# Kernel tuning notes

Hardware: AMD Instinct MI355X
Metric: run time of the kernel (lower is better)

## Reference

```python
import jax, jax.numpy as jnp
import numpy as np

N = 100_000      # n_nodes
E = 1_000_000    # n_edges (avg degree 10)
DIN = 64
DOUT = 64


def setup_inputs() -> dict:
    key = jax.random.key(0)
    k1, k2, k3, k4 = jax.random.split(key, 4)
    x = jax.random.normal(k1, (N, DIN), dtype=jnp.float32)
    edge_index = jax.random.randint(k2, (2, E), 0, N, dtype=jnp.int32)
    # GCNConv linear weight (glorot-ish scale) and bias
    W = jax.random.normal(k3, (DIN, DOUT), dtype=jnp.float32) * (1.0 / np.sqrt(DIN))
    b = jax.random.normal(k4, (DOUT,), dtype=jnp.float32) * 0.01
    return {"x": x, "edge_index": edge_index, "W": W, "b": b}


def reference(x, edge_index, W, b):
    n = x.shape[0]
    # linear transform first (PyG GCNConv: x = self.lin(x))
    h = x @ W  # [N, DOUT]
    # add self-loops
    loop = jnp.arange(n, dtype=edge_index.dtype)
    row = jnp.concatenate([edge_index[0], loop])  # source j
    col = jnp.concatenate([edge_index[1], loop])  # target i
    # symmetric normalization: deg computed on target index (PyG gcn_norm)
    deg = jax.ops.segment_sum(jnp.ones(row.shape[0], dtype=h.dtype), col, num_segments=n)
    dinv = jnp.where(deg > 0, jax.lax.rsqrt(deg), 0.0)
    norm = dinv[row] * dinv[col]  # [E+N]
    # gather source features, scale, scatter-add to targets
    out = jax.ops.segment_sum(norm[:, None] * h[row], col, num_segments=n)
    out = out + b
    # dropout is identity in eval mode; act = relu
    return jax.nn.relu(out)
```

## Files before the change

### kernel.cpp

```cpp
#include <hip/hip_runtime.h>
#include <hip/hip_bf16.h>

#define F 64
#define BK 128
#define CAP 4096
#define PA_BLOCKS 256

typedef __attribute__((ext_vector_type(8))) short bf16x8;
typedef __attribute__((ext_vector_type(4))) float f32x4;

static __device__ inline short f2bf_bits(float f) {
    union { __hip_bfloat16 b; short s; } cv;
    cv.b = __float2bfloat16(f);
    return cv.s;
}

static __device__ inline void bf8_add(uint4 u, float* a) {
    a[0] += __uint_as_float(u.x << 16);
    a[1] += __uint_as_float(u.x & 0xffff0000u);
    a[2] += __uint_as_float(u.y << 16);
    a[3] += __uint_as_float(u.y & 0xffff0000u);
    a[4] += __uint_as_float(u.z << 16);
    a[5] += __uint_as_float(u.z & 0xffff0000u);
    a[6] += __uint_as_float(u.w << 16);
    a[7] += __uint_as_float(u.w & 0xffff0000u);
}

__global__ void gemm_kernel(const float* __restrict__ x, const float* __restrict__ W,
                            __hip_bfloat16* __restrict__ h, int* __restrict__ bcursor,
                            int n) {
    __shared__ short Wb[F * F];
    int tid = threadIdx.x;
    if (blockIdx.x == 0) {
        for (int i = tid; i < 1024; i += 256) bcursor[i] = 0;
    }
    for (int i = tid; i < F * F; i += 256) Wb[i] = f2bf_bits(W[i]);
    __syncthreads();
    int lane = tid & 63;
    int wv = tid >> 6;
    int quad = lane >> 4;
    int l16 = lane & 15;

    bf16x8 bfr[2][4];
#pragma unroll
    for (int ks = 0; ks < 2; ++ks)
#pragma unroll
        for (int nb = 0; nb < 4; ++nb) {
            bf16x8 f;
#pragma unroll
            for (int j = 0; j < 8; ++j)
                f[j] = Wb[(ks * 32 + quad * 8 + j) * F + nb * 16 + l16];
            bfr[ks][nb] = f;
        }

    int blockbase = blockIdx.x * 256;
#pragma unroll
    for (int mt = 0; mt < 4; ++mt) {
        int trow = blockbase + (wv * 4 + mt) * 16;
        int ar = trow + l16;
        bf16x8 af0, af1;
        if (ar < n) {
            const float* xr = x + (size_t)ar * F + quad * 8;
            float4 v0 = ((const float4*)xr)[0];
            float4 v1 = ((const float4*)xr)[1];
            float4 v2 = ((const float4*)(xr + 32))[0];
            float4 v3 = ((const float4*)(xr + 32))[1];
            af0[0] = f2bf_bits(v0.x); af0[1] = f2bf_bits(v0.y);
            af0[2] = f2bf_bits(v0.z); af0[3] = f2bf_bits(v0.w);
            af0[4] = f2bf_bits(v1.x); af0[5] = f2bf_bits(v1.y);
            af0[6] = f2bf_bits(v1.z); af0[7] = f2bf_bits(v1.w);
            af1[0] = f2bf_bits(v2.x); af1[1] = f2bf_bits(v2.y);
            af1[2] = f2bf_bits(v2.z); af1[3] = f2bf_bits(v2.w);
            af1[4] = f2bf_bits(v3.x); af1[5] = f2bf_bits(v3.y);
            af1[6] = f2bf_bits(v3.z); af1[7] = f2bf_bits(v3.w);
        } else {
            af0 = (bf16x8)0; af1 = (bf16x8)0;
        }
        f32x4 acc[4];
#pragma unroll
        for (int nb = 0; nb < 4; ++nb) {
            acc[nb] = (f32x4)0.f;
            acc[nb] = __builtin_amdgcn_mfma_f32_16x16x32_bf16(af0, bfr[0][nb], acc[nb], 0, 0, 0);
            acc[nb] = __builtin_amdgcn_mfma_f32_16x16x32_bf16(af1, bfr[1][nb], acc[nb], 0, 0, 0);
        }
#pragma unroll
        for (int nb = 0; nb < 4; ++nb)
#pragma unroll
            for (int r = 0; r < 4; ++r) {
                int grow = trow + quad * 4 + r;
                if (grow < n)
                    h[(size_t)grow * F + nb * 16 + l16] = __float2bfloat16(acc[nb][r]);
            }
    }
}

__global__ void passA_kernel(const int* __restrict__ row, const int* __restrict__ col,
                             int* __restrict__ bcursor, unsigned* __restrict__ bin,
                             int e, int K, int chunk) {
    __shared__ int lh[1024];
    __shared__ int lbase[1024];
    int tid = threadIdx.x;
    int s = blockIdx.x * chunk;
    int lim = s + chunk;
    if (lim > e) lim = e;
    for (int i = tid; i < K; i += 256) lh[i] = 0;
    __syncthreads();
    for (int i = s + tid; i < lim; i += 256) atomicAdd(&lh[col[i] >> 7], 1);
    __syncthreads();
    for (int i = tid; i < K; i += 256) {
        int c = lh[i];
        lbase[i] = c ? atomicAdd(&bcursor[i], c) : 0;
        lh[i] = 0;
    }
    __syncthreads();
    for (int i = s + tid; i < lim; i += 256) {
        int d = col[i];
        int bkt = d >> 7;
        int off = lbase[bkt] + atomicAdd(&lh[bkt], 1);
        if (off < CAP)
            bin[(size_t)bkt * CAP + off] = ((unsigned)row[i] << 7) | ((unsigned)d & 127u);
    }
}

__global__ void passB_kernel(const unsigned* __restrict__ bin, const int* __restrict__ bcursor,
                             int* __restrict__ csr, int4* __restrict__ rng4,
                             __hip_bfloat16* __restrict__ h, int n) {
    __shared__ int lcnt[BK];
    __shared__ int lcur[BK];
    __shared__ int sc[BK];
    __shared__ float sdinv[BK];
    int tid = threadIdx.x;
    int b = blockIdx.x;
    int base = b << 7;
    int s = b * CAP;
    int cnt_all = min(bcursor[b], CAP);
    int e2 = s + cnt_all;
    if (tid < BK) lcnt[tid] = 0;
    __syncthreads();
    for (int p = s + tid; p < e2; p += 256) atomicAdd(&lcnt[bin[p] & 127u], 1);
    __syncthreads();
    if (tid < BK) sc[tid] = lcnt[tid];
    __syncthreads();
    for (int off = 1; off < BK; off <<= 1) {
        int t = (tid < BK && tid >= off) ? sc[tid - off] : 0;
        __syncthreads();
        if (tid < BK) sc[tid] += t;
        __syncthreads();
    }
    if (tid < BK) {
        int cnt = lcnt[tid];
        int lstart = sc[tid] - cnt;
        lcur[tid] = lstart;
        int node = base + tid;
        if (node < n) {
            int gs = s + lstart;
            float di = rsqrtf((float)(cnt + 1));
            rng4[node] = make_int4(gs, gs + cnt, __float_as_int(di), 0);
            sdinv[tid] = di;
        }
    }
    __syncthreads();
    for (int p = s + tid; p < e2; p += 256) {
        unsigned u = bin[p];
        int ld = (int)(u & 127u);
        int src = (int)(u >> 7);
        int pos = s + atomicAdd(&lcur[ld], 1);
        csr[pos] = src;
    }
    int lim = BK * F;
    for (int idx = tid; idx < lim; idx += 256) {
        int node = base + (idx >> 6);
        if (node < n) {
            float di = sdinv[idx >> 6];
            size_t off = (size_t)node * F + (idx & 63);
            h[off] = __float2bfloat16(di * __bfloat162float(h[off]));
        }
    }
}

__global__ void gather_kernel(const __hip_bfloat16* __restrict__ h,
                              const int* __restrict__ csr,
                              const int4* __restrict__ rng4,
                              const float* __restrict__ b,
                              float* __restrict__ out, int n) {
    int gid = blockIdx.x * 256 + threadIdx.x;
    int i = gid >> 3;
    if (i >= n) return;
    int cl = gid & 7;
    const uint4* h8 = (const uint4*)h;
    int4 r4 = rng4[i];
    int p = r4.x, pend = r4.y;
    float di = __int_as_float(r4.z);
    float acc[8] = {0.f, 0.f, 0.f, 0.f, 0.f, 0.f, 0.f, 0.f};
    bf8_add(h8[(size_t)i * 8 + cl], acc);
    for (; p + 4 <= pend; p += 4) {
        int s0 = csr[p];     int s1 = csr[p + 1];
        int s2 = csr[p + 2]; int s3 = csr[p + 3];
        uint4 u0 = h8[(size_t)s0 * 8 + cl];
        uint4 u1 = h8[(size_t)s1 * 8 + cl];
        uint4 u2 = h8[(size_t)s2 * 8 + cl];
        uint4 u3 = h8[(size_t)s3 * 8 + cl];
        bf8_add(u0, acc);
        bf8_add(u1, acc);
        bf8_add(u2, acc);
        bf8_add(u3, acc);
    }
    for (; p < pend; ++p) bf8_add(h8[(size_t)csr[p] * 8 + cl], acc);
    float4 b0 = ((const float4*)b)[cl * 2];
    float4 b1 = ((const float4*)b)[cl * 2 + 1];
    float4 r0, r1;
    r0.x = di * acc[0] + b0.x; r0.y = di * acc[1] + b0.y;
    r0.z = di * acc[2] + b0.z; r0.w = di * acc[3] + b0.w;
    r1.x = di * acc[4] + b1.x; r1.y = di * acc[5] + b1.y;
    r1.z = di * acc[6] + b1.z; r1.w = di * acc[7] + b1.w;
    r0.x = r0.x > 0.f ? r0.x : 0.f; r0.y = r0.y > 0.f ? r0.y : 0.f;
    r0.z = r0.z > 0.f ? r0.z : 0.f; r0.w = r0.w > 0.f ? r0.w : 0.f;
    r1.x = r1.x > 0.f ? r1.x : 0.f; r1.y = r1.y > 0.f ? r1.y : 0.f;
    r1.z = r1.z > 0.f ? r1.z : 0.f; r1.w = r1.w > 0.f ? r1.w : 0.f;
    ((float4*)out)[(size_t)i * 16 + cl * 2] = r0;
    ((float4*)out)[(size_t)i * 16 + cl * 2 + 1] = r1;
}

extern "C" void kernel_launch(void* const* d_in, const int* in_sizes, int n_in,
                              void* d_out, int out_size, void* d_ws, size_t ws_size,
                              hipStream_t stream) {
    const float* x = (const float*)d_in[0];
    const int* ei  = (const int*)d_in[1];
    const float* W = (const float*)d_in[2];
    const float* b = (const float*)d_in[3];
    float* out = (float*)d_out;

    int n = in_sizes[0] / F;
    int e = in_sizes[1] / 2;
    const int* row = ei;
    const int* col = ei + e;
    int K = (n + BK - 1) / BK;

    __hip_bfloat16* h = (__hip_bfloat16*)d_ws;
    unsigned* bin = (unsigned*)((char*)d_ws + (size_t)n * F * 2);
    int* csr      = (int*)(bin + (size_t)K * CAP);
    int4* rng4    = (int4*)(csr + (size_t)K * CAP);
    int* bcursor  = (int*)(rng4 + n);

    gemm_kernel<<<(n + 255) / 256, 256, 0, stream>>>(x, W, h, bcursor, n);

    int chunk = (e + PA_BLOCKS - 1) / PA_BLOCKS;
    passA_kernel<<<PA_BLOCKS, 256, 0, stream>>>(row, col, bcursor, bin, e, K, chunk);

    passB_kernel<<<K, 256, 0, stream>>>(bin, bcursor, csr, rng4, h, n);

    gather_kernel<<<((size_t)n * 8 + 255) / 256, 256, 0, stream>>>(
        h, csr, rng4, b, out, n);
}
```

Measured before the change: 151.9 us.

## Merge GEMM with binning pass and replace CSR build with LDS-atomic bucket scatter

GEMM blocks and edge-binning blocks now run inside one launch as heterogeneous blocks, and the cursor reset moves to a memset. The CSR construction pass is removed. A small per-bucket kernel computes dinv, and a per-bucket gather kernel accumulates dinv-weighted neighbor features directly into a padded shared-memory tile with float atomics. This drops the CSR write/read and the in-place rescale of h. The cost is heavy LDS atomic traffic (8 atomics per thread per edge), an extra global dinv lookup per edge, and only K≈782 blocks with large LDS use in the gather stage.

```diff
diff --git a/kernel.cpp b/kernel.cpp
--- a/kernel.cpp
+++ b/kernel.cpp
@@ -5,6 +5,7 @@
 #define BK 128
 #define CAP 4096
 #define PA_BLOCKS 256
+#define STRIDE 65
 
 typedef __attribute__((ext_vector_type(8))) short bf16x8;
 typedef __attribute__((ext_vector_type(4))) float f32x4;
@@ -15,210 +16,168 @@
     return cv.s;
 }
 
-static __device__ inline void bf8_add(uint4 u, float* a) {
-    a[0] += __uint_as_float(u.x << 16);
-    a[1] += __uint_as_float(u.x & 0xffff0000u);
-    a[2] += __uint_as_float(u.y << 16);
-    a[3] += __uint_as_float(u.y & 0xffff0000u);
-    a[4] += __uint_as_float(u.z << 16);
-    a[5] += __uint_as_float(u.z & 0xffff0000u);
-    a[6] += __uint_as_float(u.w << 16);
-    a[7] += __uint_as_float(u.w & 0xffff0000u);
-}
-
-__global__ void gemm_kernel(const float* __restrict__ x, const float* __restrict__ W,
-                            __hip_bfloat16* __restrict__ h, int* __restrict__ bcursor,
-                            int n) {
-    __shared__ short Wb[F * F];
+__global__ void __launch_bounds__(256)
+k1_kernel(const float* __restrict__ x, const float* __restrict__ W,
+          __hip_bfloat16* __restrict__ h,
+          const int* __restrict__ row, const int* __restrict__ col,
+          int* __restrict__ bcursor, unsigned* __restrict__ bin,
+          int n, int e, int ngemm, int K, int chunk) {
+    __shared__ int smem[2048];
     int tid = threadIdx.x;
-    if (blockIdx.x == 0) {
-        for (int i = tid; i < 1024; i += 256) bcursor[i] = 0;
-    }
-    for (int i = tid; i < F * F; i += 256) Wb[i] = f2bf_bits(W[i]);
-    __syncthreads();
-    int lane = tid & 63;
-    int wv = tid >> 6;
-    int quad = lane >> 4;
-    int l16 = lane & 15;
-
-    bf16x8 bfr[2][4];
-#pragma unroll
-    for (int ks = 0; ks < 2; ++ks)
-#pragma unroll
-        for (int nb = 0; nb < 4; ++nb) {
-            bf16x8 f;
-#pragma unroll
-            for (int j = 0; j < 8; ++j)
-                f[j] = Wb[(ks * 32 + quad * 8 + j) * F + nb * 16 + l16];
-            bfr[ks][nb] = f;
-        }
-
-    int blockbase = blockIdx.x * 256;
-#pragma unroll
-    for (int mt = 0; mt < 4; ++mt) {
-        int trow = blockbase + (wv * 4 + mt) * 16;
-        int ar = trow + l16;
-        bf16x8 af0, af1;
-        if (ar < n) {
-            const float* xr = x + (size_t)ar * F + quad * 8;
-            float4 v0 = ((const float4*)xr)[0];
-            float4 v1 = ((const float4*)xr)[1];
-            float4 v2 = ((const float4*)(xr + 32))[0];
-            float4 v3 = ((const float4*)(xr + 32))[1];
-            af0[0] = f2bf_bits(v0.x); af0[1] = f2bf_bits(v0.y);
-            af0[2] = f2bf_bits(v0.z); af0[3] = f2bf_bits(v0.w);
-            af0[4] = f2bf_bits(v1.x); af0[5] = f2bf_bits(v1.y);
-            af0[6] = f2bf_bits(v1.z); af0[7] = f2bf_bits(v1.w);
-            af1[0] = f2bf_bits(v2.x); af1[1] = f2bf_bits(v2.y);
-            af1[2] = f2bf_bits(v2.z); af1[3] = f2bf_bits(v2.w);
-            af1[4] = f2bf_bits(v3.x); af1[5] = f2bf_bits(v3.y);
-            af1[6] = f2bf_bits(v3.z); af1[7] = f2bf_bits(v3.w);
-        } else {
-            af0 = (bf16x8)0; af1 = (bf16x8)0;
-        }
-        f32x4 acc[4];
-#pragma unroll
-        for (int nb = 0; nb < 4; ++nb) {
-            acc[nb] = (f32x4)0.f;
-            acc[nb] = __builtin_amdgcn_mfma_f32_16x16x32_bf16(af0, bfr[0][nb], acc[nb], 0, 0, 0);
-            acc[nb] = __builtin_amdgcn_mfma_f32_16x16x32_bf16(af1, bfr[1][nb], acc[nb], 0, 0, 0);
-        }
-#pragma unroll
-        for (int nb = 0; nb < 4; ++nb)
-#pragma unroll
-            for (int r = 0; r < 4; ++r) {
-                int grow = trow + quad * 4 + r;
-                if (grow < n)
-                    h[(size_t)grow * F + nb * 16 + l16] = __float2bfloat16(acc[nb][r]);
+
+    if ((int)blockIdx.x < ngemm) {
+        short* Wb = (short*)smem;
+        for (int i = tid; i < F * F; i += 256) Wb[i] = f2bf_bits(W[i]);
+        __syncthreads();
+        int lane = tid & 63;
+        int wv = tid >> 6;
+        int quad = lane >> 4;
+        int l16 = lane & 15;
+
+        bf16x8 bfr[2][4];
+#pragma unroll
+        for (int ks = 0; ks < 2; ++ks)
+#pragma unroll
+            for (int nb = 0; nb < 4; ++nb) {
+                bf16x8 f;
+#pragma unroll
+                for (int j = 0; j < 8; ++j)
+                    f[j] = Wb[(ks * 32 + quad * 8 + j) * F + nb * 16 + l16];
+                bfr[ks][nb] = f;
             }
-    }
-}
-
-__global__ void passA_kernel(const int* __restrict__ row, const int* __restrict__ col,
-                             int* __restrict__ bcursor, unsigned* __restrict__ bin,
-                             int e, int K, int chunk) {
-    __shared__ int lh[1024];
-    __shared__ int lbase[1024];
+
+        int blockbase = blockIdx.x * 256;
+#pragma unroll
+        for (int mt = 0; mt < 4; ++mt) {
+            int trow = blockbase + (wv * 4 + mt) * 16;
+            int ar = trow + l16;
+            bf16x8 af0, af1;
+            if (ar < n) {
+                const float* xr = x + (size_t)ar * F + quad * 8;
+                float4 v0 = ((const float4*)xr)[0];
+                float4 v1 = ((const float4*)xr)[1];
+                float4 v2 = ((const float4*)(xr + 32))[0];
+                float4 v3 = ((const float4*)(xr + 32))[1];
+                af0[0] = f2bf_bits(v0.x); af0[1] = f2bf_bits(v0.y);
+                af0[2] = f2bf_bits(v0.z); af0[3] = f2bf_bits(v0.w);
+                af0[4] = f2bf_bits(v1.x); af0[5] = f2bf_bits(v1.y);
+                af0[6] = f2bf_bits(v1.z); af0[7] = f2bf_bits(v1.w);
+                af1[0] = f2bf_bits(v2.x); af1[1] = f2bf_bits(v2.y);
+                af1[2] = f2bf_bits(v2.z); af1[3] = f2bf_bits(v2.w);
+                af1[4] = f2bf_bits(v3.x); af1[5] = f2bf_bits(v3.y);
+                af1[6] = f2bf_bits(v3.z); af1[7] = f2bf_bits(v3.w);
+            } else {
+                af0 = (bf16x8)0; af1 = (bf16x8)0;
+            }
+            f32x4 acc[4];
+#pragma unroll
+            for (int nb = 0; nb < 4; ++nb) {
+                acc[nb] = (f32x4)0.f;
+                acc[nb] = __builtin_amdgcn_mfma_f32_16x16x32_bf16(af0, bfr[0][nb], acc[nb], 0, 0, 0);
+                acc[nb] = __builtin_amdgcn_mfma_f32_16x16x32_bf16(af1, bfr[1][nb], acc[nb], 0, 0, 0);
+            }
+#pragma unroll
+            for (int nb = 0; nb < 4; ++nb)
+#pragma unroll
+                for (int r = 0; r < 4; ++r) {
+                    int grow = trow + quad * 4 + r;
+                    if (grow < n)
+                        h[(size_t)grow * F + nb * 16 + l16] = __float2bfloat16(acc[nb][r]);
+                }
+        }
+    } else {
+        int* lh = smem;
+        int* lbase = smem + 1024;
+        int pb = blockIdx.x - ngemm;
+        int s = pb * chunk;
+        int lim = min(s + chunk, e);
+        for (int i = tid; i < K; i += 256) lh[i] = 0;
+        __syncthreads();
+        for (int i = s + tid; i < lim; i += 256) atomicAdd(&lh[col[i] >> 7], 1);
+        __syncthreads();
+        for (int i = tid; i < K; i += 256) {
+            int c = lh[i];
+            lbase[i] = c ? atomicAdd(&bcursor[i], c) : 0;
+            lh[i] = 0;
+        }
+        __syncthreads();
+        for (int i = s + tid; i < lim; i += 256) {
+            int d = col[i];
+            int bkt = d >> 7;
+            int off = lbase[bkt] + atomicAdd(&lh[bkt], 1);
+            if (off < CAP)
+                bin[(size_t)bkt * CAP + off] = ((unsigned)row[i] << 7) | ((unsigned)d & 127u);
+        }
+    }
+}
+
+__global__ void __launch_bounds__(256)
+dinv_kernel(const unsigned* __restrict__ bin, const int* __restrict__ bcursor,
+            float* __restrict__ dinv, int n) {
+    __shared__ int lcnt[BK];
     int tid = threadIdx.x;
-    int s = blockIdx.x * chunk;
-    int lim = s + chunk;
-    if (lim > e) lim = e;
-    for (int i = tid; i < K; i += 256) lh[i] = 0;
-    __syncthreads();
-    for (int i = s + tid; i < lim; i += 256) atomicAdd(&lh[col[i] >> 7], 1);
-    __syncthreads();
-    for (int i = tid; i < K; i += 256) {
-        int c = lh[i];
-        lbase[i] = c ? atomicAdd(&bcursor[i], c) : 0;
-        lh[i] = 0;
-    }
-    __syncthreads();
-    for (int i = s + tid; i < lim; i += 256) {
-        int d = col[i];
-        int bkt = d >> 7;
-        int off = lbase[bkt] + atomicAdd(&lh[bkt], 1);
-        if (off < CAP)
-            bin[(size_t)bkt * CAP + off] = ((unsigned)row[i] << 7) | ((unsigned)d & 127u);
-    }
-}
-
-__global__ void passB_kernel(const unsigned* __restrict__ bin, const int* __restrict__ bcursor,
-                             int* __restrict__ csr, int4* __restrict__ rng4,
-                             __hip_bfloat16* __restrict__ h, int n) {
-    __shared__ int lcnt[BK];
-    __shared__ int lcur[BK];
-    __shared__ int sc[BK];
-    __shared__ float sdinv[BK];
+    int b = blockIdx.x;
+    int s = b * CAP;
+    int cnt = min(bcursor[b], CAP);
+    if (tid < BK) lcnt[tid] = 0;
+    __syncthreads();
+    for (int p = tid; p < cnt; p += 256) atomicAdd(&lcnt[bin[s + p] & 127u], 1);
+    __syncthreads();
+    if (tid < BK) {
+        int node = (b << 7) + tid;
+        if (node < n) dinv[node] = rsqrtf((float)(lcnt[tid] + 1));
+    }
+}
+
+__global__ void __launch_bounds__(256)
+gather_kernel(const unsigned* __restrict__ bin, const int* __restrict__ bcursor,
+              const float* __restrict__ dinv, const __hip_bfloat16* __restrict__ h,
+              const float* __restrict__ bias, float* __restrict__ out, int n) {
+    __shared__ float acc[BK * STRIDE];
     int tid = threadIdx.x;
     int b = blockIdx.x;
     int base = b << 7;
     int s = b * CAP;
-    int cnt_all = min(bcursor[b], CAP);
-    int e2 = s + cnt_all;
-    if (tid < BK) lcnt[tid] = 0;
-    __syncthreads();
-    for (int p = s + tid; p < e2; p += 256) atomicAdd(&lcnt[bin[p] & 127u], 1);
-    __syncthreads();
-    if (tid < BK) sc[tid] = lcnt[tid];
-    __syncthreads();
-    for (int off = 1; off < BK; off <<= 1) {
-        int t = (tid < BK && tid >= off) ? sc[tid - off] : 0;
-        __syncthreads();
-        if (tid < BK) sc[tid] += t;
-        __syncthreads();
-    }
-    if (tid < BK) {
-        int cnt = lcnt[tid];
-        int lstart = sc[tid] - cnt;
-        lcur[tid] = lstart;
-        int node = base + tid;
+    int cnt = min(bcursor[b], CAP);
+
+    for (int idx = tid; idx < BK * F; idx += 256) {
+        int ln = idx >> 6, ch = idx & 63;
+        int node = base + ln;
+        float v = 0.f;
+        if (node < n) v = dinv[node] * __bfloat162float(h[(size_t)node * F + ch]);
+        acc[ln * STRIDE + ch] = v;
+    }
+    __syncthreads();
+
+    int g = tid >> 3, cl = tid & 7;
+    const uint4* h8 = (const uint4*)h;
+    for (int p = g; p < cnt; p += 32) {
+        unsigned u = bin[s + p];
+        int src = (int)(u >> 7);
+        int ld = (int)(u & 127u);
+        float w = dinv[src];
+        uint4 hv = h8[(size_t)src * 8 + cl];
+        float* a = &acc[ld * STRIDE + cl * 8];
+        atomicAdd(a + 0, w * __uint_as_float(hv.x << 16));
+        atomicAdd(a + 1, w * __uint_as_float(hv.x & 0xffff0000u));
+        atomicAdd(a + 2, w * __uint_as_float(hv.y << 16));
+        atomicAdd(a + 3, w * __uint_as_float(hv.y & 0xffff0000u));
+        atomicAdd(a + 4, w * __uint_as_float(hv.z << 16));
+        atomicAdd(a + 5, w * __uint_as_float(hv.z & 0xffff0000u));
+        atomicAdd(a + 6, w * __uint_as_float(hv.w << 16));
+        atomicAdd(a + 7, w * __uint_as_float(hv.w & 0xffff0000u));
+    }
+    __syncthreads();
+
+    for (int idx = tid; idx < BK * F; idx += 256) {
+        int ln = idx >> 6, ch = idx & 63;
+        int node = base + ln;
         if (node < n) {
-            int gs = s + lstart;
-            float di = rsqrtf((float)(cnt + 1));
-            rng4[node] = make_int4(gs, gs + cnt, __float_as_int(di), 0);
-            sdinv[tid] = di;
-        }
-    }
-    __syncthreads();
-    for (int p = s + tid; p < e2; p += 256) {
-        unsigned u = bin[p];
-        int ld = (int)(u & 127u);
-        int src = (int)(u >> 7);
-        int pos = s + atomicAdd(&lcur[ld], 1);
-        csr[pos] = src;
-    }
-    int lim = BK * F;
-    for (int idx = tid; idx < lim; idx += 256) {
-        int node = base + (idx >> 6);
-        if (node < n) {
-            float di = sdinv[idx >> 6];
-            size_t off = (size_t)node * F + (idx & 63);
-            h[off] = __float2bfloat16(di * __bfloat162float(h[off]));
-        }
-    }
-}
-
-__global__ void gather_kernel(const __hip_bfloat16* __restrict__ h,
-                              const int* __restrict__ csr,
-                              const int4* __restrict__ rng4,
-                              const float* __restrict__ b,
-                              float* __restrict__ out, int n) {
-    int gid = blockIdx.x * 256 + threadIdx.x;
-    int i = gid >> 3;
-    if (i >= n) return;
-    int cl = gid & 7;
-    const uint4* h8 = (const uint4*)h;
-    int4 r4 = rng4[i];
-    int p = r4.x, pend = r4.y;
-    float di = __int_as_float(r4.z);
-    float acc[8] = {0.f, 0.f, 0.f, 0.f, 0.f, 0.f, 0.f, 0.f};
-    bf8_add(h8[(size_t)i * 8 + cl], acc);
-    for (; p + 4 <= pend; p += 4) {
-        int s0 = csr[p];     int s1 = csr[p + 1];
-        int s2 = csr[p + 2]; int s3 = csr[p + 3];
-        uint4 u0 = h8[(size_t)s0 * 8 + cl];
-        uint4 u1 = h8[(size_t)s1 * 8 + cl];
-        uint4 u2 = h8[(size_t)s2 * 8 + cl];
-        uint4 u3 = h8[(size_t)s3 * 8 + cl];
-        bf8_add(u0, acc);
-        bf8_add(u1, acc);
-        bf8_add(u2, acc);
-        bf8_add(u3, acc);
-    }
-    for (; p < pend; ++p) bf8_add(h8[(size_t)csr[p] * 8 + cl], acc);
-    float4 b0 = ((const float4*)b)[cl * 2];
-    float4 b1 = ((const float4*)b)[cl * 2 + 1];
-    float4 r0, r1;
-    r0.x = di * acc[0] + b0.x; r0.y = di * acc[1] + b0.y;
-    r0.z = di * acc[2] + b0.z; r0.w = di * acc[3] + b0.w;
-    r1.x = di * acc[4] + b1.x; r1.y = di * acc[5] + b1.y;
-    r1.z = di * acc[6] + b1.z; r1.w = di * acc[7] + b1.w;
-    r0.x = r0.x > 0.f ? r0.x : 0.f; r0.y = r0.y > 0.f ? r0.y : 0.f;
-    r0.z = r0.z > 0.f ? r0.z : 0.f; r0.w = r0.w > 0.f ? r0.w : 0.f;
-    r1.x = r1.x > 0.f ? r1.x : 0.f; r1.y = r1.y > 0.f ? r1.y : 0.f;
-    r1.z = r1.z > 0.f ? r1.z : 0.f; r1.w = r1.w > 0.f ? r1.w : 0.f;
-    ((float4*)out)[(size_t)i * 16 + cl * 2] = r0;
-    ((float4*)out)[(size_t)i * 16 + cl * 2 + 1] = r1;
+            float di = dinv[node];
+            float v = di * acc[ln * STRIDE + ch] + bias[ch];
+            out[(size_t)node * F + ch] = v > 0.f ? v : 0.f;
+        }
+    }
 }
 
 extern "C" void kernel_launch(void* const* d_in, const int* in_sizes, int n_in,
@@ -238,17 +197,17 @@
 
     __hip_bfloat16* h = (__hip_bfloat16*)d_ws;
     unsigned* bin = (unsigned*)((char*)d_ws + (size_t)n * F * 2);
-    int* csr      = (int*)(bin + (size_t)K * CAP);
-    int4* rng4    = (int4*)(csr + (size_t)K * CAP);
-    int* bcursor  = (int*)(rng4 + n);
-
-    gemm_kernel<<<(n + 255) / 256, 256, 0, stream>>>(x, W, h, bcursor, n);
-
+    float* dinv   = (float*)(bin + (size_t)K * CAP);
+    int* bcursor  = (int*)(dinv + n);
+
+    hipMemsetAsync(bcursor, 0, 1024 * sizeof(int), stream);
+
+    int ngemm = (n + 255) / 256;
     int chunk = (e + PA_BLOCKS - 1) / PA_BLOCKS;
-    passA_kernel<<<PA_BLOCKS, 256, 0, stream>>>(row, col, bcursor, bin, e, K, chunk);
-
-    passB_kernel<<<K, 256, 0, stream>>>(bin, bcursor, csr, rng4, h, n);
-
-    gather_kernel<<<((size_t)n * 8 + 255) / 256, 256, 0, stream>>>(
-        h, csr, rng4, b, out, n);
-}
+    k1_kernel<<<ngemm + PA_BLOCKS, 256, 0, stream>>>(x, W, h, row, col, bcursor,
+                                                     bin, n, e, ngemm, K, chunk);
+
+    dinv_kernel<<<K, 256, 0, stream>>>(bin, bcursor, dinv, n);
+
+    gather_kernel<<<K, 256, 0, stream>>>(bin, bcursor, dinv, h, b, out, n);
+}
```

Result: slower. 545.7 us (+259.3%).
